# Kernel tuning notes

Measured on AMD Instinct MI355X. Metric: run time of the kernel, lower is better.

Reference implementation:

```python
import jax, jax.numpy as jnp
import numpy as np

D_MODEL = 768
DT_RANK = D_MODEL // 16  # 48
D_CONV = 4
D_INNER = 2 * D_MODEL    # 1536
D_STATE = 16
BATCH, SEQ_LEN = 1, 4096


def setup_inputs() -> dict:
    key = jax.random.key(0)
    ks = jax.random.split(key, 11)
    def n(k, shape, scale=0.02):
        return jax.random.normal(k, shape, dtype=jnp.float32) * scale
    return {
        "u": jax.random.normal(ks[0], (BATCH, SEQ_LEN, D_MODEL), dtype=jnp.float32),
        "in_proj_w": n(ks[1], (2 * D_INNER, D_MODEL)),
        "conv_w": n(ks[2], (D_INNER, 1, D_CONV)),
        "conv_b": n(ks[3], (D_INNER,)),
        "x_dt_w": n(ks[4], (DT_RANK, D_INNER)),
        "x_b_w": n(ks[5], (D_STATE, D_INNER)),
        "x_c_w": n(ks[6], (D_STATE, D_INNER)),
        "dt_w": n(ks[7], (D_INNER, DT_RANK)),
        "dt_b": n(ks[8], (D_INNER,)),
        # HF Mamba-style S4D-real init: A_log = log(1..N) per channel
        "A_log": jnp.log(jnp.tile(jnp.arange(1, D_STATE + 1, dtype=jnp.float32), (D_INNER, 1))),
        "D_param": jnp.ones((D_INNER,), dtype=jnp.float32),
        "out_proj_w": n(ks[9], (D_MODEL, D_INNER)),
    }


def _silu(x):
    return x * jax.nn.sigmoid(x)


def reference(u, in_proj_w, conv_w, conv_b, x_dt_w, x_b_w, x_c_w,
              dt_w, dt_b, A_log, D_param, out_proj_w):
    batch = u.shape[0]
    # input projection -> x, z  [B, L, D_INNER] each
    xz = u @ in_proj_w.T
    x, z = jnp.split(xz, 2, axis=-1)
    # causal depthwise conv1d over time
    x_ncl = jnp.transpose(x, (0, 2, 1))  # [B, D_INNER, L]
    x_conv = jax.lax.conv_general_dilated(
        x_ncl, conv_w, window_strides=(1,), padding=[(D_CONV - 1, 0)],
        dimension_numbers=("NCH", "OIH", "NCH"), feature_group_count=D_INNER)
    x_conv = x_conv + conv_b[None, :, None]
    x_conv = _silu(jnp.transpose(x_conv, (0, 2, 1)))  # [B, L, D_INNER]
    # data-dependent SSM parameters
    dt_rank = x_conv @ x_dt_w.T                      # [B, L, DT_RANK]
    Bm = x_conv @ x_b_w.T                            # [B, L, D_STATE]
    Cm = x_conv @ x_c_w.T                            # [B, L, D_STATE]
    dt = jax.nn.softplus(dt_rank @ dt_w.T + dt_b)    # [B, L, D_INNER]
    A = -jnp.exp(A_log)                              # [D_INNER, D_STATE]
    dA = jnp.exp(dt[..., None] * A)                  # [B, L, D_INNER, D_STATE]
    dB = dt[..., None] * Bm[:, :, None, :]           # [B, L, D_INNER, D_STATE]

    def step(h, inp):
        dA_t, dB_t, x_t, C_t = inp
        h = h * dA_t + x_t[..., None] * dB_t                 # [B, D_INNER, D_STATE]
        y_t = jnp.sum(h * C_t[:, None, :], axis=-1) + D_param * x_t
        return h, y_t

    h0 = jnp.zeros((batch, D_INNER, D_STATE), dtype=u.dtype)
    scan_inputs = (jnp.moveaxis(dA, 1, 0), jnp.moveaxis(dB, 1, 0),
                   jnp.moveaxis(x_conv, 1, 0), jnp.moveaxis(Cm, 1, 0))
    _, y_ssm = jax.lax.scan(step, h0, scan_inputs)   # [L, B, D_INNER]
    y = jnp.moveaxis(y_ssm, 0, 1) * _silu(z)         # [B, L, D_INNER]
    return y @ out_proj_w.T                          # [B, L, D_MODEL]
```

## Files before the change

### kernel.cpp

```cpp
#include <hip/hip_runtime.h>
#include <math.h>

#define L      4096
#define DM     768
#define DI     1536
#define DS     16
#define DR     48
#define NCOMB  80
#define CH     16
#define NC     256
#define G2_S   16
#define G2_KC  96
#define XZROW  6144

typedef unsigned short u16;
typedef unsigned int   u32;
typedef __attribute__((ext_vector_type(8))) short bf16x8;
typedef __attribute__((ext_vector_type(4))) float f32x4;

__device__ __forceinline__ float silu_f(float v) { return v / (1.f + __expf(-v)); }

__device__ __forceinline__ u16 f2bf(float f) {
    u32 u = __float_as_uint(f);
    return (u16)((u + 0x7fffu + ((u >> 16) & 1u)) >> 16);
}
__device__ __forceinline__ float bf2f(u16 h) {
    return __uint_as_float(((u32)h) << 16);
}

__device__ __forceinline__ float softplus_f(float s) {
    return (s > 20.f) ? s : log1pf(expf(s));
}

__device__ __forceinline__ void gl_lds16(const u16* g, u16* l) {
    __builtin_amdgcn_global_load_lds(
        (const __attribute__((address_space(1))) void*)g,
        (__attribute__((address_space(3))) void*)l, 16, 0, 0);
}

__global__ __launch_bounds__(256)
void gemm_bf16_bt(const u16* __restrict__ A, const u16* __restrict__ W,
                  float* __restrict__ C, int M, int N, int K)
{
    __shared__ u16 As[2][128 * 32];
    __shared__ u16 Bs[2][128 * 32];

    const int tid  = threadIdx.x;
    const int lane = tid & 63;
    const int wave = tid >> 6;
    const int wr   = (wave >> 1) * 64;
    const int wc   = (wave & 1) * 64;
    const int m0   = blockIdx.y * 128;
    const int n0   = blockIdx.x * 128;

    const int r0 = tid >> 2;
    const int k0 = (tid & 3) * 8;

    const int frow = lane & 15;
    const int fk   = (lane >> 4) * 8;

    f32x4 acc[4][4];
    #pragma unroll
    for (int i = 0; i < 4; ++i)
        #pragma unroll
        for (int j = 0; j < 4; ++j)
            acc[i][j] = (f32x4){0.f, 0.f, 0.f, 0.f};

    const int NT = K >> 5;

#define STAGE(buf, kk) {                                                       \
        const u16* ga = A + (size_t)(m0 + r0) * K + (kk) + k0;                 \
        const u16* gw = W + (size_t)(n0 + r0) * K + (kk) + k0;                 \
        gl_lds16(ga,                   &As[buf][tid * 8]);                     \
        gl_lds16(ga + (size_t)64 * K,  &As[buf][2048 + tid * 8]);              \
        gl_lds16(gw,                   &Bs[buf][tid * 8]);                     \
        gl_lds16(gw + (size_t)64 * K,  &Bs[buf][2048 + tid * 8]); }

    STAGE(0, 0);
    __syncthreads();

    for (int t = 0; t < NT; ++t) {
        const int b = t & 1;
        if (t + 1 < NT) STAGE(b ^ 1, (t + 1) << 5);

        bf16x8 af[4], bw[4];
        #pragma unroll
        for (int m = 0; m < 4; ++m)
            af[m] = *(const bf16x8*)&As[b][(wr + m * 16 + frow) * 32 + fk];
        #pragma unroll
        for (int n = 0; n < 4; ++n)
            bw[n] = *(const bf16x8*)&Bs[b][(wc + n * 16 + frow) * 32 + fk];

        #pragma unroll
        for (int m = 0; m < 4; ++m)
            #pragma unroll
            for (int n = 0; n < 4; ++n)
                acc[m][n] = __builtin_amdgcn_mfma_f32_16x16x32_bf16(
                    af[m], bw[n], acc[m][n], 0, 0, 0);

        __syncthreads();
    }
#undef STAGE

    const int crow = (lane >> 4) * 4;
    const int ccol = lane & 15;
    #pragma unroll
    for (int m = 0; m < 4; ++m)
        #pragma unroll
        for (int n = 0; n < 4; ++n)
            #pragma unroll
            for (int r = 0; r < 4; ++r)
                C[(size_t)(m0 + wr + m * 16 + crow + r) * N
                  + n0 + wc + n * 16 + ccol] = acc[m][n][r];
}

__global__ __launch_bounds__(256)
void gemm_bf16_bt_n64(const u16* __restrict__ A, int lda,
                      const u16* __restrict__ W, int ldw,
                      float* __restrict__ C, int M, int N, int K)
{
    __shared__ u16 As[2][128 * 32];
    __shared__ u16 Bs[2][64 * 32];

    const int tid  = threadIdx.x;
    const int lane = tid & 63;
    const int wave = tid >> 6;
    const int wr   = (wave >> 1) * 64;
    const int wc   = (wave & 1) * 32;
    const int m0   = blockIdx.y * 128;
    const int n0   = blockIdx.x * 64;

    const int r0 = tid >> 2;
    const int k0 = (tid & 3) * 8;

    const int frow = lane & 15;
    const int fk   = (lane >> 4) * 8;

    f32x4 acc[4][2];
    #pragma unroll
    for (int i = 0; i < 4; ++i)
        #pragma unroll
        for (int j = 0; j < 2; ++j)
            acc[i][j] = (f32x4){0.f, 0.f, 0.f, 0.f};

    const int NT = K >> 5;

#define STG(buf, kk) {                                                         \
        const u16* ga = A + (size_t)(m0 + r0) * lda + (kk) + k0;               \
        gl_lds16(ga,                     &As[buf][tid * 8]);                   \
        gl_lds16(ga + (size_t)64 * lda,  &As[buf][2048 + tid * 8]);            \
        gl_lds16(W + (size_t)(n0 + r0) * ldw + (kk) + k0, &Bs[buf][tid * 8]); }

    STG(0, 0);
    __syncthreads();

    for (int t = 0; t < NT; ++t) {
        const int b = t & 1;
        if (t + 1 < NT) STG(b ^ 1, (t + 1) << 5);

        bf16x8 af[4], bw[2];
        #pragma unroll
        for (int m = 0; m < 4; ++m)
            af[m] = *(const bf16x8*)&As[b][(wr + m * 16 + frow) * 32 + fk];
        #pragma unroll
        for (int n = 0; n < 2; ++n)
            bw[n] = *(const bf16x8*)&Bs[b][(wc + n * 16 + frow) * 32 + fk];

        #pragma unroll
        for (int m = 0; m < 4; ++m)
            #pragma unroll
            for (int n = 0; n < 2; ++n)
                acc[m][n] = __builtin_amdgcn_mfma_f32_16x16x32_bf16(
                    af[m], bw[n], acc[m][n], 0, 0, 0);

        __syncthreads();
    }
#undef STG

    const int crow = (lane >> 4) * 4;
    const int ccol = lane & 15;
    #pragma unroll
    for (int m = 0; m < 4; ++m)
        #pragma unroll
        for (int n = 0; n < 2; ++n)
            #pragma unroll
            for (int r = 0; r < 4; ++r)
                C[(size_t)(m0 + wr + m * 16 + crow + r) * N
                  + n0 + wc + n * 16 + ccol] = acc[m][n][r];
}

#define NU4  (L * DM / 4)
#define NW4  (2 * DI * DM / 4)
#define NWT  (DI * NCOMB)
__global__ __launch_bounds__(256)
void pack_early_k(const float* __restrict__ u, const float* __restrict__ Wip,
                  const float* __restrict__ xdt, const float* __restrict__ xb,
                  const float* __restrict__ xc,
                  u16* __restrict__ ubf, u16* __restrict__ Wipb,
                  float* __restrict__ Wt)
{
    int i = blockIdx.x * 256 + threadIdx.x;
    if (i < NU4) {
        const float4 v = ((const float4*)u)[i];
        ushort4 o; o.x = f2bf(v.x); o.y = f2bf(v.y); o.z = f2bf(v.z); o.w = f2bf(v.w);
        ((ushort4*)ubf)[i] = o;
        return;
    }
    i -= NU4;
    if (i < NW4) {
        const float4 v = ((const float4*)Wip)[i];
        ushort4 o; o.x = f2bf(v.x); o.y = f2bf(v.y); o.z = f2bf(v.z); o.w = f2bf(v.w);
        ((ushort4*)Wipb)[i] = o;
        return;
    }
    i -= NW4;
    if (i < NWT) {
        const int k = i / NCOMB, n = i - k * NCOMB;
        float v;
        if (n < 48)      v = xdt[n * DI + k];
        else if (n < 64) v = xb[(n - 48) * DI + k];
        else             v = xc[(n - 64) * DI + k];
        Wt[i] = v;
    }
}

#define NO4  (DM * DI / 4)
__global__ __launch_bounds__(256)
void pack_wop_k(const float* __restrict__ Wop, u16* __restrict__ xzu)
{
    int i = blockIdx.x * 256 + threadIdx.x;
    if (i >= NO4) return;
    const float4 v = ((const float4*)Wop)[i];
    ushort4 o; o.x = f2bf(v.x); o.y = f2bf(v.y); o.z = f2bf(v.z); o.w = f2bf(v.w);
    const int e = i * 4;
    const int r = e / DI, c = e - r * DI;
    *(ushort4*)(xzu + (size_t)r * XZROW + 1536 + c) = o;
}

__global__ __launch_bounds__(256)
void conv_silu_v4(const float* __restrict__ xz, const float* __restrict__ cw,
                  const float* __restrict__ cb, float* __restrict__ xcv)
{
    int idx = blockIdx.x * 256 + threadIdx.x;
    if (idx >= L * (DI / 4)) return;
    const int t = idx / (DI / 4);
    const int q = idx - t * (DI / 4);
    const int d = q * 4;

    const float4 w0 = ((const float4*)cw)[d + 0];
    const float4 w1 = ((const float4*)cw)[d + 1];
    const float4 w2 = ((const float4*)cw)[d + 2];
    const float4 w3 = ((const float4*)cw)[d + 3];
    float4 acc = ((const float4*)cb)[q];

    const float* base = xz + d;
    #pragma unroll
    for (int j = 0; j < 4; ++j) {
        const int tt = t - 3 + j;
        if (tt >= 0) {
            const float4 x = *(const float4*)(base + (size_t)tt * (2 * DI));
            acc.x = fmaf(((const float*)&w0)[j], x.x, acc.x);
            acc.y = fmaf(((const float*)&w1)[j], x.y, acc.y);
            acc.z = fmaf(((const float*)&w2)[j], x.z, acc.z);
            acc.w = fmaf(((const float*)&w3)[j], x.w, acc.w);
        }
    }
    float4 o;
    o.x = silu_f(acc.x); o.y = silu_f(acc.y);
    o.z = silu_f(acc.z); o.w = silu_f(acc.w);
    ((float4*)xcv)[idx] = o;
}

__global__ __launch_bounds__(256)
void gemm2_splitk(const float* __restrict__ A, const float* __restrict__ Wt,
                  float* __restrict__ part)
{
    __shared__ float As[G2_KC][65];
    __shared__ float Ws[G2_KC][80];

    const int tid  = threadIdx.x;
    const int m0   = blockIdx.x * 64;
    const int koff = blockIdx.y * G2_KC;

    {
        const int r = tid >> 2, cg = tid & 3;
        #pragma unroll
        for (int j = 0; j < 6; ++j) {
            const int kk = (j * 4 + cg) * 4;
            const float4 v = *(const float4*)(A + (size_t)(m0 + r) * DI + koff + kk);
            As[kk + 0][r] = v.x; As[kk + 1][r] = v.y;
            As[kk + 2][r] = v.z; As[kk + 3][r] = v.w;
        }
    }
    for (int i = tid; i < G2_KC * 80; i += 256)
        (&Ws[0][0])[i] = Wt[(size_t)koff * 80 + i];
    __syncthreads();

    const int g  = tid >> 6;
    const int r  = tid & 63;
    const int c0 = g * 20;

    float acc[20];
    #pragma unroll
    for (int j = 0; j < 20; ++j) acc[j] = 0.f;

    #pragma unroll 2
    for (int k = 0; k < G2_KC; ++k) {
        const float a = As[k][r];
        #pragma unroll
        for (int q = 0; q < 5; ++q) {
            const float4 w = *(const float4*)&Ws[k][c0 + q * 4];
            acc[q * 4 + 0] = fmaf(a, w.x, acc[q * 4 + 0]);
            acc[q * 4 + 1] = fmaf(a, w.y, acc[q * 4 + 1]);
            acc[q * 4 + 2] = fmaf(a, w.z, acc[q * 4 + 2]);
            acc[q * 4 + 3] = fmaf(a, w.w, acc[q * 4 + 3]);
        }
    }

    float* p = part + (size_t)blockIdx.y * (L * NCOMB)
                    + (size_t)(m0 + r) * NCOMB + c0;
    #pragma unroll
    for (int q = 0; q < 5; ++q)
        ((float4*)p)[q] = make_float4(acc[q * 4], acc[q * 4 + 1],
                                      acc[q * 4 + 2], acc[q * 4 + 3]);
}

__global__ __launch_bounds__(256)
void gemm2_reduce(const float* __restrict__ part, float* __restrict__ dtbc)
{
    int i = blockIdx.x * 256 + threadIdx.x;
    if (i >= L * NCOMB) return;
    float s = 0.f;
    #pragma unroll
    for (int j = 0; j < G2_S; ++j)
        s += part[(size_t)j * L * NCOMB + i];
    dtbc[i] = s;
}

__global__ __launch_bounds__(256)
void dt_k(const float* __restrict__ dtbc, const float* __restrict__ dtw,
          const float* __restrict__ dtb, u16* __restrict__ dt)
{
    __shared__ float dtr_s[32][48];
    const int tid = threadIdx.x;
    const int d   = blockIdx.x * 256 + tid;
    const int t0  = blockIdx.y * 32;

    for (int i = tid; i < 384; i += 256) {
        const int r = i / 12, c = (i - r * 12) * 4;
        const float4 v = *(const float4*)(dtbc + (size_t)(t0 + r) * NCOMB + c);
        *(float4*)&dtr_s[r][c] = v;
    }
    __syncthreads();

    float w[48];
    #pragma unroll
    for (int j = 0; j < 12; ++j) {
        const float4 v = *(const float4*)(dtw + (size_t)d * DR + j * 4);
        w[j * 4 + 0] = v.x; w[j * 4 + 1] = v.y;
        w[j * 4 + 2] = v.z; w[j * 4 + 3] = v.w;
    }
    const float b = dtb[d];

    for (int t = 0; t < 32; ++t) {
        float s = b;
        #pragma unroll
        for (int j = 0; j < 12; ++j) {
            const float4 v = *(const float4*)&dtr_s[t][j * 4];
            s = fmaf(v.x, w[j * 4 + 0], s);
            s = fmaf(v.y, w[j * 4 + 1], s);
            s = fmaf(v.z, w[j * 4 + 2], s);
            s = fmaf(v.w, w[j * 4 + 3], s);
        }
        dt[(size_t)(t0 + t) * DI + d] = f2bf(softplus_f(s));
    }
}

__global__ __launch_bounds__(256)
void scan1_k(const u16* __restrict__ dt, const float* __restrict__ xcv,
             const float* __restrict__ dtbc, const float* __restrict__ alog,
             u16* __restrict__ hloc, float* __restrict__ Ssum)
{
    __shared__ float Bs[CH][DS];
    const int c = blockIdx.y;
    const int d = blockIdx.x * 256 + threadIdx.x;

    {
        const int i = threadIdx.x;
        const int tt = i >> 4, n = i & 15;
        Bs[tt][n] = dtbc[(size_t)(c * CH + tt) * NCOMB + 48 + n];
    }
    __syncthreads();

    float Ad[DS], h[DS];
    #pragma unroll
    for (int n = 0; n < DS; ++n) {
        Ad[n] = -expf(alog[d * DS + n]);
        h[n] = 0.f;
    }

    size_t base = (size_t)(c * CH) * DI + d;
    float S = 0.f;
    for (int tt = 0; tt < CH; ++tt, base += DI) {
        const float dtv = bf2f(dt[base]);
        const float xv  = xcv[base];
        S += dtv;
        const float xdt = xv * dtv;
        #pragma unroll
        for (int n = 0; n < DS; ++n)
            h[n] = fmaf(h[n], __expf(Ad[n] * dtv), xdt * Bs[tt][n]);
    }

    u16* o = hloc + ((size_t)c * DI + d) * DS;
    #pragma unroll
    for (int q = 0; q < 4; ++q) {
        ushort4 pk;
        pk.x = f2bf(h[q * 4 + 0]); pk.y = f2bf(h[q * 4 + 1]);
        pk.z = f2bf(h[q * 4 + 2]); pk.w = f2bf(h[q * 4 + 3]);
        *(ushort4*)(o + q * 4) = pk;
    }
    Ssum[c * DI + d] = S;
}

__global__ __launch_bounds__(256)
void scan2_k(u16* hc, const float* __restrict__ Ssum,
             const float* __restrict__ alog)
{
    const int p = blockIdx.x * 256 + threadIdx.x;
    if (p >= DI * DS) return;
    const int d = p >> 4;
    const float Ad = -expf(alog[p]);
    float h = 0.f;
    for (int c = 0; c < NC; ++c) {
        const size_t o = (size_t)c * DI * DS + p;
        const float hl = bf2f(hc[o]);
        hc[o] = f2bf(h);
        h = fmaf(h, __expf(Ad * Ssum[c * DI + d]), hl);
    }
}

__global__ __launch_bounds__(256)
void scan3_k(const u16* __restrict__ dt, const float* __restrict__ xcv,
             const float* __restrict__ dtbc, const float* __restrict__ alog,
             const u16* __restrict__ carry, const float* __restrict__ Dp,
             const float* __restrict__ xz, u16* __restrict__ ybf)
{
    __shared__ float Bs[CH][DS];
    __shared__ float Cs[CH][DS];
    const int c = blockIdx.y;
    const int d = blockIdx.x * 256 + threadIdx.x;

    {
        const int i = threadIdx.x;
        const int tt = i >> 4, n = i & 15;
        Bs[tt][n] = dtbc[(size_t)(c * CH + tt) * NCOMB + 48 + n];
        Cs[tt][n] = dtbc[(size_t)(c * CH + tt) * NCOMB + 64 + n];
    }
    __syncthreads();

    float Ad[DS], h[DS];
    const u16* co = carry + ((size_t)c * DI + d) * DS;
    #pragma unroll
    for (int q = 0; q < 4; ++q) {
        const ushort4 cv = *(const ushort4*)(co + q * 4);
        h[q * 4 + 0] = bf2f(cv.x); h[q * 4 + 1] = bf2f(cv.y);
        h[q * 4 + 2] = bf2f(cv.z); h[q * 4 + 3] = bf2f(cv.w);
    }
    #pragma unroll
    for (int n = 0; n < DS; ++n)
        Ad[n] = -expf(alog[d * DS + n]);
    const float Dv = Dp[d];

    int t = c * CH;
    for (int tt = 0; tt < CH; ++tt, ++t) {
        const size_t o = (size_t)t * DI + d;
        const float dtv = bf2f(dt[o]);
        const float xv  = xcv[o];
        const float xdt = xv * dtv;
        float y = Dv * xv;
        #pragma unroll
        for (int n = 0; n < DS; ++n) {
            h[n] = fmaf(h[n], __expf(Ad[n] * dtv), xdt * Bs[tt][n]);
            y = fmaf(h[n], Cs[tt][n], y);
        }
        const float z = xz[(size_t)t * (2 * DI) + DI + d];
        ybf[(size_t)t * XZROW + d] = f2bf(y * silu_f(z));
    }
}

extern "C" void kernel_launch(void* const* d_in, const int* in_sizes, int n_in,
                              void* d_out, int out_size, void* d_ws, size_t ws_size,
                              hipStream_t stream)
{
    const float* u    = (const float*)d_in[0];
    const float* Wip  = (const float*)d_in[1];
    const float* cw   = (const float*)d_in[2];
    const float* cb   = (const float*)d_in[3];
    const float* xdt  = (const float*)d_in[4];
    const float* xbw  = (const float*)d_in[5];
    const float* xcw  = (const float*)d_in[6];
    const float* dtw  = (const float*)d_in[7];
    const float* dtb  = (const float*)d_in[8];
    const float* alog = (const float*)d_in[9];
    const float* Dp   = (const float*)d_in[10];
    const float* Wop  = (const float*)d_in[11];
    float* out = (float*)d_out;

    float* ws   = (float*)d_ws;
    float* xz   = ws;
    float* xcv  = xz   + (size_t)L * 2 * DI;
    float* dtbc = xcv  + (size_t)L * DI;
    float* dty  = dtbc + (size_t)L * NCOMB;
    float* Wt   = dty  + (size_t)L * DI;
    u16*   hc   = (u16*)(Wt + (size_t)DI * NCOMB);
    float* Ssum = Wt + (size_t)DI * NCOMB
                     + (size_t)NC * DI * DS / 2;

    u16*   ubf  = (u16*)xcv;
    u16*   Wipb = (u16*)xcv + (size_t)L * DM;
    float* g2p  = dty;
    u16*   dtbf = (u16*)dty;
    u16*   xzu  = (u16*)xz;

    const dim3 blk(256);

    pack_early_k<<<(NU4 + NW4 + NWT + 255) / 256, blk, 0, stream>>>(
        u, Wip, xdt, xbw, xcw, ubf, Wipb, Wt);

    gemm_bf16_bt<<<dim3((2 * DI) / 128, L / 128), blk, 0, stream>>>(
        ubf, Wipb, xz, L, 2 * DI, DM);

    conv_silu_v4<<<(L * (DI / 4) + 255) / 256, blk, 0, stream>>>(xz, cw, cb, xcv);

    pack_wop_k<<<(NO4 + 255) / 256, blk, 0, stream>>>(Wop, xzu);

    gemm2_splitk<<<dim3(L / 64, G2_S), blk, 0, stream>>>(xcv, Wt, g2p);
    gemm2_reduce<<<(L * NCOMB + 255) / 256, blk, 0, stream>>>(g2p, dtbc);

    dt_k<<<dim3(DI / 256, L / 32), blk, 0, stream>>>(dtbc, dtw, dtb, dtbf);

    scan1_k<<<dim3(DI / 256, NC), blk, 0, stream>>>(
        dtbf, xcv, dtbc, alog, hc, Ssum);
    scan2_k<<<(DI * DS) / 256, blk, 0, stream>>>(hc, Ssum, alog);
    scan3_k<<<dim3(DI / 256, NC), blk, 0, stream>>>(
        dtbf, xcv, dtbc, alog, hc, Dp, xz, xzu);

    gemm_bf16_bt_n64<<<dim3(DM / 64, L / 128), blk, 0, stream>>>(
        xzu, XZROW, xzu + 1536, XZROW, out, L, DM, DI);
}
```

Baseline: 247.9 us.

## Process two channels per thread in chunked scan and precompute negated A

The chunk-local scan kernels (scan1, scan3) now have each thread handle two adjacent channels, using paired loads of dt, x, z and packed stores, and halving the grid. -exp(A_log) is computed once in the packing kernel into a workspace buffer and read as float4s instead of being recomputed in every scan block. This aims to cut redundant exp work and per-element load instructions and to increase ILP. The cost is twice the state registers per thread and fewer blocks: 3x256 in each chunked scan kernel.

```diff
diff --git a/kernel.cpp b/kernel.cpp
--- a/kernel.cpp
+++ b/kernel.cpp
@@ -192,12 +192,13 @@
 #define NU4  (L * DM / 4)
 #define NW4  (2 * DI * DM / 4)
 #define NWT  (DI * NCOMB)
+#define NA   (DI * DS)
 __global__ __launch_bounds__(256)
 void pack_early_k(const float* __restrict__ u, const float* __restrict__ Wip,
                   const float* __restrict__ xdt, const float* __restrict__ xb,
-                  const float* __restrict__ xc,
+                  const float* __restrict__ xc, const float* __restrict__ alog,
                   u16* __restrict__ ubf, u16* __restrict__ Wipb,
-                  float* __restrict__ Wt)
+                  float* __restrict__ Wt, float* __restrict__ Aneg)
 {
     int i = blockIdx.x * 256 + threadIdx.x;
     if (i < NU4) {
@@ -221,7 +222,11 @@
         else if (n < 64) v = xb[(n - 48) * DI + k];
         else             v = xc[(n - 64) * DI + k];
         Wt[i] = v;
-    }
+        return;
+    }
+    i -= NWT;
+    if (i < NA)
+        Aneg[i] = -expf(alog[i]);
 }
 
 #define NO4  (DM * DI / 4)
@@ -378,58 +383,69 @@
 
 __global__ __launch_bounds__(256)
 void scan1_k(const u16* __restrict__ dt, const float* __restrict__ xcv,
-             const float* __restrict__ dtbc, const float* __restrict__ alog,
+             const float* __restrict__ dtbc, const float* __restrict__ Aneg,
              u16* __restrict__ hloc, float* __restrict__ Ssum)
 {
     __shared__ float Bs[CH][DS];
+    const int tid = threadIdx.x;
     const int c = blockIdx.y;
-    const int d = blockIdx.x * 256 + threadIdx.x;
+    const int d = blockIdx.x * 512 + 2 * tid;
 
     {
-        const int i = threadIdx.x;
-        const int tt = i >> 4, n = i & 15;
+        const int tt = tid >> 4, n = tid & 15;
         Bs[tt][n] = dtbc[(size_t)(c * CH + tt) * NCOMB + 48 + n];
     }
     __syncthreads();
 
-    float Ad[DS], h[DS];
-    #pragma unroll
-    for (int n = 0; n < DS; ++n) {
-        Ad[n] = -expf(alog[d * DS + n]);
-        h[n] = 0.f;
-    }
+    float Ad0[DS], Ad1[DS], h0[DS], h1[DS];
+    #pragma unroll
+    for (int q = 0; q < 4; ++q) {
+        *(float4*)&Ad0[q * 4] = *(const float4*)(Aneg + (size_t)d * DS + q * 4);
+        *(float4*)&Ad1[q * 4] = *(const float4*)(Aneg + (size_t)(d + 1) * DS + q * 4);
+    }
+    #pragma unroll
+    for (int n = 0; n < DS; ++n) { h0[n] = 0.f; h1[n] = 0.f; }
 
     size_t base = (size_t)(c * CH) * DI + d;
-    float S = 0.f;
+    float S0 = 0.f, S1 = 0.f;
     for (int tt = 0; tt < CH; ++tt, base += DI) {
-        const float dtv = bf2f(dt[base]);
-        const float xv  = xcv[base];
-        S += dtv;
-        const float xdt = xv * dtv;
-        #pragma unroll
-        for (int n = 0; n < DS; ++n)
-            h[n] = fmaf(h[n], __expf(Ad[n] * dtv), xdt * Bs[tt][n]);
+        const u32 dtp = *(const u32*)(dt + base);
+        const float dtv0 = bf2f((u16)(dtp & 0xffff));
+        const float dtv1 = bf2f((u16)(dtp >> 16));
+        const float2 xv = *(const float2*)(xcv + base);
+        S0 += dtv0; S1 += dtv1;
+        const float xdt0 = xv.x * dtv0;
+        const float xdt1 = xv.y * dtv1;
+        #pragma unroll
+        for (int n = 0; n < DS; ++n) {
+            const float b = Bs[tt][n];
+            h0[n] = fmaf(h0[n], __expf(Ad0[n] * dtv0), xdt0 * b);
+            h1[n] = fmaf(h1[n], __expf(Ad1[n] * dtv1), xdt1 * b);
+        }
     }
 
     u16* o = hloc + ((size_t)c * DI + d) * DS;
     #pragma unroll
     for (int q = 0; q < 4; ++q) {
         ushort4 pk;
-        pk.x = f2bf(h[q * 4 + 0]); pk.y = f2bf(h[q * 4 + 1]);
-        pk.z = f2bf(h[q * 4 + 2]); pk.w = f2bf(h[q * 4 + 3]);
+        pk.x = f2bf(h0[q * 4 + 0]); pk.y = f2bf(h0[q * 4 + 1]);
+        pk.z = f2bf(h0[q * 4 + 2]); pk.w = f2bf(h0[q * 4 + 3]);
         *(ushort4*)(o + q * 4) = pk;
-    }
-    Ssum[c * DI + d] = S;
+        pk.x = f2bf(h1[q * 4 + 0]); pk.y = f2bf(h1[q * 4 + 1]);
+        pk.z = f2bf(h1[q * 4 + 2]); pk.w = f2bf(h1[q * 4 + 3]);
+        *(ushort4*)(o + DS + q * 4) = pk;
+    }
+    *(float2*)(Ssum + (size_t)c * DI + d) = make_float2(S0, S1);
 }
 
 __global__ __launch_bounds__(256)
 void scan2_k(u16* hc, const float* __restrict__ Ssum,
-             const float* __restrict__ alog)
+             const float* __restrict__ Aneg)
 {
     const int p = blockIdx.x * 256 + threadIdx.x;
     if (p >= DI * DS) return;
     const int d = p >> 4;
-    const float Ad = -expf(alog[p]);
+    const float Ad = Aneg[p];
     float h = 0.f;
     for (int c = 0; c < NC; ++c) {
         const size_t o = (size_t)c * DI * DS + p;
@@ -441,50 +457,65 @@
 
 __global__ __launch_bounds__(256)
 void scan3_k(const u16* __restrict__ dt, const float* __restrict__ xcv,
-             const float* __restrict__ dtbc, const float* __restrict__ alog,
+             const float* __restrict__ dtbc, const float* __restrict__ Aneg,
              const u16* __restrict__ carry, const float* __restrict__ Dp,
              const float* __restrict__ xz, u16* __restrict__ ybf)
 {
     __shared__ float Bs[CH][DS];
     __shared__ float Cs[CH][DS];
+    const int tid = threadIdx.x;
     const int c = blockIdx.y;
-    const int d = blockIdx.x * 256 + threadIdx.x;
+    const int d = blockIdx.x * 512 + 2 * tid;
 
     {
-        const int i = threadIdx.x;
-        const int tt = i >> 4, n = i & 15;
+        const int tt = tid >> 4, n = tid & 15;
         Bs[tt][n] = dtbc[(size_t)(c * CH + tt) * NCOMB + 48 + n];
         Cs[tt][n] = dtbc[(size_t)(c * CH + tt) * NCOMB + 64 + n];
     }
     __syncthreads();
 
-    float Ad[DS], h[DS];
+    float Ad0[DS], Ad1[DS], h0[DS], h1[DS];
+    #pragma unroll
+    for (int q = 0; q < 4; ++q) {
+        *(float4*)&Ad0[q * 4] = *(const float4*)(Aneg + (size_t)d * DS + q * 4);
+        *(float4*)&Ad1[q * 4] = *(const float4*)(Aneg + (size_t)(d + 1) * DS + q * 4);
+    }
     const u16* co = carry + ((size_t)c * DI + d) * DS;
     #pragma unroll
     for (int q = 0; q < 4; ++q) {
-        const ushort4 cv = *(const ushort4*)(co + q * 4);
-        h[q * 4 + 0] = bf2f(cv.x); h[q * 4 + 1] = bf2f(cv.y);
-        h[q * 4 + 2] = bf2f(cv.z); h[q * 4 + 3] = bf2f(cv.w);
-    }
-    #pragma unroll
-    for (int n = 0; n < DS; ++n)
-        Ad[n] = -expf(alog[d * DS + n]);
-    const float Dv = Dp[d];
+        ushort4 cv = *(const ushort4*)(co + q * 4);
+        h0[q * 4 + 0] = bf2f(cv.x); h0[q * 4 + 1] = bf2f(cv.y);
+        h0[q * 4 + 2] = bf2f(cv.z); h0[q * 4 + 3] = bf2f(cv.w);
+        cv = *(const ushort4*)(co + DS + q * 4);
+        h1[q * 4 + 0] = bf2f(cv.x); h1[q * 4 + 1] = bf2f(cv.y);
+        h1[q * 4 + 2] = bf2f(cv.z); h1[q * 4 + 3] = bf2f(cv.w);
+    }
+    const float2 Dv = *(const float2*)(Dp + d);
 
     int t = c * CH;
     for (int tt = 0; tt < CH; ++tt, ++t) {
         const size_t o = (size_t)t * DI + d;
-        const float dtv = bf2f(dt[o]);
-        const float xv  = xcv[o];
-        const float xdt = xv * dtv;
-        float y = Dv * xv;
+        const u32 dtp = *(const u32*)(dt + o);
+        const float dtv0 = bf2f((u16)(dtp & 0xffff));
+        const float dtv1 = bf2f((u16)(dtp >> 16));
+        const float2 xv = *(const float2*)(xcv + o);
+        const float xdt0 = xv.x * dtv0;
+        const float xdt1 = xv.y * dtv1;
+        float y0 = Dv.x * xv.x;
+        float y1 = Dv.y * xv.y;
         #pragma unroll
         for (int n = 0; n < DS; ++n) {
-            h[n] = fmaf(h[n], __expf(Ad[n] * dtv), xdt * Bs[tt][n]);
-            y = fmaf(h[n], Cs[tt][n], y);
+            const float b = Bs[tt][n];
+            const float cc = Cs[tt][n];
+            h0[n] = fmaf(h0[n], __expf(Ad0[n] * dtv0), xdt0 * b);
+            h1[n] = fmaf(h1[n], __expf(Ad1[n] * dtv1), xdt1 * b);
+            y0 = fmaf(h0[n], cc, y0);
+            y1 = fmaf(h1[n], cc, y1);
         }
-        const float z = xz[(size_t)t * (2 * DI) + DI + d];
-        ybf[(size_t)t * XZROW + d] = f2bf(y * silu_f(z));
+        const float2 z = *(const float2*)(xz + (size_t)t * (2 * DI) + DI + d);
+        const u32 pk = (u32)f2bf(y0 * silu_f(z.x))
+                     | ((u32)f2bf(y1 * silu_f(z.y)) << 16);
+        *(u32*)(ybf + (size_t)t * XZROW + d) = pk;
     }
 }
 
@@ -515,6 +546,7 @@
     u16*   hc   = (u16*)(Wt + (size_t)DI * NCOMB);
     float* Ssum = Wt + (size_t)DI * NCOMB
                      + (size_t)NC * DI * DS / 2;
+    float* Aneg = Ssum + (size_t)NC * DI;
 
     u16*   ubf  = (u16*)xcv;
     u16*   Wipb = (u16*)xcv + (size_t)L * DM;
@@ -524,8 +556,8 @@
 
     const dim3 blk(256);
 
-    pack_early_k<<<(NU4 + NW4 + NWT + 255) / 256, blk, 0, stream>>>(
-        u, Wip, xdt, xbw, xcw, ubf, Wipb, Wt);
+    pack_early_k<<<(NU4 + NW4 + NWT + NA + 255) / 256, blk, 0, stream>>>(
+        u, Wip, xdt, xbw, xcw, alog, ubf, Wipb, Wt, Aneg);
 
     gemm_bf16_bt<<<dim3((2 * DI) / 128, L / 128), blk, 0, stream>>>(
         ubf, Wipb, xz, L, 2 * DI, DM);
@@ -539,11 +571,11 @@
 
     dt_k<<<dim3(DI / 256, L / 32), blk, 0, stream>>>(dtbc, dtw, dtb, dtbf);
 
-    scan1_k<<<dim3(DI / 256, NC), blk, 0, stream>>>(
-        dtbf, xcv, dtbc, alog, hc, Ssum);
-    scan2_k<<<(DI * DS) / 256, blk, 0, stream>>>(hc, Ssum, alog);
-    scan3_k<<<dim3(DI / 256, NC), blk, 0, stream>>>(
-        dtbf, xcv, dtbc, alog, hc, Dp, xz, xzu);
+    scan1_k<<<dim3(DI / 512, NC), blk, 0, stream>>>(
+        dtbf, xcv, dtbc, Aneg, hc, Ssum);
+    scan2_k<<<(DI * DS) / 256, blk, 0, stream>>>(hc, Ssum, Aneg);
+    scan3_k<<<dim3(DI / 512, NC), blk, 0, stream>>>(
+        dtbf, xcv, dtbc, Aneg, hc, Dp, xz, xzu);
 
     gemm_bf16_bt_n64<<<dim3(DM / 64, L / 128), blk, 0, stream>>>(
         xzu, XZROW, xzu + 1536, XZROW, out, L, DM, DI);
```

Result: no change. 252.2 us (+1.7%).

## Fuse three-pass chunked scan into one cooperative kernel with grid syncs

Applied to the files above, without the earlier changes.

Merges the three scan kernels (per-chunk local scan, cross-chunk carry propagation, final output pass) into one cooperative kernel separated by grid-wide syncs. Each chunk's dt and x values stay in shared memory between pass one and pass three instead of being reloaded from global memory. The chunk length doubles so the 768-block grid can be co-resident, and -exp(A_log) is precomputed once in the pack kernel. The risks are grid.sync overhead, a carry pass that only uses 16 of 128 chunk rows, a longer serial loop per chunk, and heavier shared-memory use that could limit occupancy.

```diff
diff --git a/kernel.cpp b/kernel.cpp
--- a/kernel.cpp
+++ b/kernel.cpp
@@ -1,4 +1,5 @@
 #include <hip/hip_runtime.h>
+#include <hip/hip_cooperative_groups.h>
 #include <math.h>
 
 #define L      4096
@@ -7,8 +8,8 @@
 #define DS     16
 #define DR     48
 #define NCOMB  80
-#define CH     16
-#define NC     256
+#define CH     32
+#define NC     128
 #define G2_S   16
 #define G2_KC  96
 #define XZROW  6144
@@ -192,12 +193,13 @@
 #define NU4  (L * DM / 4)
 #define NW4  (2 * DI * DM / 4)
 #define NWT  (DI * NCOMB)
+#define NA   (DI * DS)
 __global__ __launch_bounds__(256)
 void pack_early_k(const float* __restrict__ u, const float* __restrict__ Wip,
                   const float* __restrict__ xdt, const float* __restrict__ xb,
-                  const float* __restrict__ xc,
+                  const float* __restrict__ xc, const float* __restrict__ alog,
                   u16* __restrict__ ubf, u16* __restrict__ Wipb,
-                  float* __restrict__ Wt)
+                  float* __restrict__ Wt, float* __restrict__ Aneg)
 {
     int i = blockIdx.x * 256 + threadIdx.x;
     if (i < NU4) {
@@ -221,7 +223,11 @@
         else if (n < 64) v = xb[(n - 48) * DI + k];
         else             v = xc[(n - 64) * DI + k];
         Wt[i] = v;
-    }
+        return;
+    }
+    i -= NWT;
+    if (i < NA)
+        Aneg[i] = -expf(alog[i]);
 }
 
 #define NO4  (DM * DI / 4)
@@ -376,115 +382,116 @@
     }
 }
 
-__global__ __launch_bounds__(256)
-void scan1_k(const u16* __restrict__ dt, const float* __restrict__ xcv,
-             const float* __restrict__ dtbc, const float* __restrict__ alog,
-             u16* __restrict__ hloc, float* __restrict__ Ssum)
-{
-    __shared__ float Bs[CH][DS];
-    const int c = blockIdx.y;
-    const int d = blockIdx.x * 256 + threadIdx.x;
+namespace cg = cooperative_groups;
+
+__global__ __launch_bounds__(256)
+void scan_fused_k(const u16* __restrict__ dt, const float* __restrict__ xcv,
+                  const float* __restrict__ dtbc, const float* __restrict__ Aneg,
+                  const float* __restrict__ Dp, const float* __restrict__ xz,
+                  u16* __restrict__ ybf, u16* hc, float* __restrict__ Ssum)
+{
+    __shared__ float xs[CH][256];
+    __shared__ u16   dts[CH][256];
+
+    cg::grid_group grid = cg::this_grid();
+
+    const int tid = threadIdx.x;
+    const int cb  = blockIdx.x;
+    const int c   = blockIdx.y;
+    const int d   = cb * 256 + tid;
+
+    float Ad[DS], h[DS];
+    #pragma unroll
+    for (int q = 0; q < 4; ++q)
+        *(float4*)&Ad[q * 4] = *(const float4*)(Aneg + (size_t)d * DS + q * 4);
+    #pragma unroll
+    for (int n = 0; n < DS; ++n) h[n] = 0.f;
 
     {
-        const int i = threadIdx.x;
-        const int tt = i >> 4, n = i & 15;
-        Bs[tt][n] = dtbc[(size_t)(c * CH + tt) * NCOMB + 48 + n];
-    }
-    __syncthreads();
-
-    float Ad[DS], h[DS];
-    #pragma unroll
-    for (int n = 0; n < DS; ++n) {
-        Ad[n] = -expf(alog[d * DS + n]);
-        h[n] = 0.f;
-    }
-
-    size_t base = (size_t)(c * CH) * DI + d;
-    float S = 0.f;
-    for (int tt = 0; tt < CH; ++tt, base += DI) {
-        const float dtv = bf2f(dt[base]);
-        const float xv  = xcv[base];
-        S += dtv;
-        const float xdt = xv * dtv;
-        #pragma unroll
-        for (int n = 0; n < DS; ++n)
-            h[n] = fmaf(h[n], __expf(Ad[n] * dtv), xdt * Bs[tt][n]);
-    }
-
-    u16* o = hloc + ((size_t)c * DI + d) * DS;
-    #pragma unroll
-    for (int q = 0; q < 4; ++q) {
-        ushort4 pk;
-        pk.x = f2bf(h[q * 4 + 0]); pk.y = f2bf(h[q * 4 + 1]);
-        pk.z = f2bf(h[q * 4 + 2]); pk.w = f2bf(h[q * 4 + 3]);
-        *(ushort4*)(o + q * 4) = pk;
-    }
-    Ssum[c * DI + d] = S;
-}
-
-__global__ __launch_bounds__(256)
-void scan2_k(u16* hc, const float* __restrict__ Ssum,
-             const float* __restrict__ alog)
-{
-    const int p = blockIdx.x * 256 + threadIdx.x;
-    if (p >= DI * DS) return;
-    const int d = p >> 4;
-    const float Ad = -expf(alog[p]);
-    float h = 0.f;
-    for (int c = 0; c < NC; ++c) {
-        const size_t o = (size_t)c * DI * DS + p;
-        const float hl = bf2f(hc[o]);
-        hc[o] = f2bf(h);
-        h = fmaf(h, __expf(Ad * Ssum[c * DI + d]), hl);
-    }
-}
-
-__global__ __launch_bounds__(256)
-void scan3_k(const u16* __restrict__ dt, const float* __restrict__ xcv,
-             const float* __restrict__ dtbc, const float* __restrict__ alog,
-             const u16* __restrict__ carry, const float* __restrict__ Dp,
-             const float* __restrict__ xz, u16* __restrict__ ybf)
-{
-    __shared__ float Bs[CH][DS];
-    __shared__ float Cs[CH][DS];
-    const int c = blockIdx.y;
-    const int d = blockIdx.x * 256 + threadIdx.x;
+        size_t base = (size_t)(c * CH) * DI + d;
+        float S = 0.f;
+        for (int tt = 0; tt < CH; ++tt, base += DI) {
+            const u16  draw = dt[base];
+            const float xv  = xcv[base];
+            dts[tt][tid] = draw;
+            xs[tt][tid]  = xv;
+            const float dtv = bf2f(draw);
+            S += dtv;
+            const float xdt = xv * dtv;
+            const float* brow = dtbc + (size_t)(c * CH + tt) * NCOMB + 48;
+            #pragma unroll
+            for (int q = 0; q < 4; ++q) {
+                const float4 bq = *(const float4*)(brow + q * 4);
+                h[q * 4 + 0] = fmaf(h[q * 4 + 0], __expf(Ad[q * 4 + 0] * dtv), xdt * bq.x);
+                h[q * 4 + 1] = fmaf(h[q * 4 + 1], __expf(Ad[q * 4 + 1] * dtv), xdt * bq.y);
+                h[q * 4 + 2] = fmaf(h[q * 4 + 2], __expf(Ad[q * 4 + 2] * dtv), xdt * bq.z);
+                h[q * 4 + 3] = fmaf(h[q * 4 + 3], __expf(Ad[q * 4 + 3] * dtv), xdt * bq.w);
+            }
+        }
+        u16* o = hc + ((size_t)c * DI + d) * DS;
+        #pragma unroll
+        for (int q = 0; q < 4; ++q) {
+            ushort4 pk;
+            pk.x = f2bf(h[q * 4 + 0]); pk.y = f2bf(h[q * 4 + 1]);
+            pk.z = f2bf(h[q * 4 + 2]); pk.w = f2bf(h[q * 4 + 3]);
+            *(ushort4*)(o + q * 4) = pk;
+        }
+        Ssum[(size_t)c * DI + d] = S;
+    }
+
+    __threadfence();
+    grid.sync();
+
+    if (c < 16) {
+        const int p = (c * 6 + cb) * 256 + tid;
+        const int d2 = p >> 4;
+        const float Ad2 = Aneg[p];
+        float h2 = 0.f;
+        for (int cc = 0; cc < NC; ++cc) {
+            const size_t o = (size_t)cc * DI * DS + p;
+            const float hl = bf2f(hc[o]);
+            hc[o] = f2bf(h2);
+            h2 = fmaf(h2, __expf(Ad2 * Ssum[(size_t)cc * DI + d2]), hl);
+        }
+    }
+
+    __threadfence();
+    grid.sync();
 
     {
-        const int i = threadIdx.x;
-        const int tt = i >> 4, n = i & 15;
-        Bs[tt][n] = dtbc[(size_t)(c * CH + tt) * NCOMB + 48 + n];
-        Cs[tt][n] = dtbc[(size_t)(c * CH + tt) * NCOMB + 64 + n];
-    }
-    __syncthreads();
-
-    float Ad[DS], h[DS];
-    const u16* co = carry + ((size_t)c * DI + d) * DS;
-    #pragma unroll
-    for (int q = 0; q < 4; ++q) {
-        const ushort4 cv = *(const ushort4*)(co + q * 4);
-        h[q * 4 + 0] = bf2f(cv.x); h[q * 4 + 1] = bf2f(cv.y);
-        h[q * 4 + 2] = bf2f(cv.z); h[q * 4 + 3] = bf2f(cv.w);
-    }
-    #pragma unroll
-    for (int n = 0; n < DS; ++n)
-        Ad[n] = -expf(alog[d * DS + n]);
-    const float Dv = Dp[d];
-
-    int t = c * CH;
-    for (int tt = 0; tt < CH; ++tt, ++t) {
-        const size_t o = (size_t)t * DI + d;
-        const float dtv = bf2f(dt[o]);
-        const float xv  = xcv[o];
-        const float xdt = xv * dtv;
-        float y = Dv * xv;
-        #pragma unroll
-        for (int n = 0; n < DS; ++n) {
-            h[n] = fmaf(h[n], __expf(Ad[n] * dtv), xdt * Bs[tt][n]);
-            y = fmaf(h[n], Cs[tt][n], y);
-        }
-        const float z = xz[(size_t)t * (2 * DI) + DI + d];
-        ybf[(size_t)t * XZROW + d] = f2bf(y * silu_f(z));
+        const u16* co = hc + ((size_t)c * DI + d) * DS;
+        #pragma unroll
+        for (int q = 0; q < 4; ++q) {
+            const ushort4 cv = *(const ushort4*)(co + q * 4);
+            h[q * 4 + 0] = bf2f(cv.x); h[q * 4 + 1] = bf2f(cv.y);
+            h[q * 4 + 2] = bf2f(cv.z); h[q * 4 + 3] = bf2f(cv.w);
+        }
+        const float Dv = Dp[d];
+
+        int t = c * CH;
+        for (int tt = 0; tt < CH; ++tt, ++t) {
+            const float dtv = bf2f(dts[tt][tid]);
+            const float xv  = xs[tt][tid];
+            const float xdt = xv * dtv;
+            float y = Dv * xv;
+            const float* brow = dtbc + (size_t)(c * CH + tt) * NCOMB + 48;
+            const float* crow = brow + 16;
+            #pragma unroll
+            for (int q = 0; q < 4; ++q) {
+                const float4 bq = *(const float4*)(brow + q * 4);
+                const float4 cq = *(const float4*)(crow + q * 4);
+                h[q * 4 + 0] = fmaf(h[q * 4 + 0], __expf(Ad[q * 4 + 0] * dtv), xdt * bq.x);
+                h[q * 4 + 1] = fmaf(h[q * 4 + 1], __expf(Ad[q * 4 + 1] * dtv), xdt * bq.y);
+                h[q * 4 + 2] = fmaf(h[q * 4 + 2], __expf(Ad[q * 4 + 2] * dtv), xdt * bq.z);
+                h[q * 4 + 3] = fmaf(h[q * 4 + 3], __expf(Ad[q * 4 + 3] * dtv), xdt * bq.w);
+                y = fmaf(h[q * 4 + 0], cq.x, y);
+                y = fmaf(h[q * 4 + 1], cq.y, y);
+                y = fmaf(h[q * 4 + 2], cq.z, y);
+                y = fmaf(h[q * 4 + 3], cq.w, y);
+            }
+            const float z = xz[(size_t)t * (2 * DI) + DI + d];
+            ybf[(size_t)t * XZROW + d] = f2bf(y * silu_f(z));
+        }
     }
 }
 
@@ -515,6 +522,7 @@
     u16*   hc   = (u16*)(Wt + (size_t)DI * NCOMB);
     float* Ssum = Wt + (size_t)DI * NCOMB
                      + (size_t)NC * DI * DS / 2;
+    float* Aneg = Ssum + (size_t)NC * DI;
 
     u16*   ubf  = (u16*)xcv;
     u16*   Wipb = (u16*)xcv + (size_t)L * DM;
@@ -524,8 +532,8 @@
 
     const dim3 blk(256);
 
-    pack_early_k<<<(NU4 + NW4 + NWT + 255) / 256, blk, 0, stream>>>(
-        u, Wip, xdt, xbw, xcw, ubf, Wipb, Wt);
+    pack_early_k<<<(NU4 + NW4 + NWT + NA + 255) / 256, blk, 0, stream>>>(
+        u, Wip, xdt, xbw, xcw, alog, ubf, Wipb, Wt, Aneg);
 
     gemm_bf16_bt<<<dim3((2 * DI) / 128, L / 128), blk, 0, stream>>>(
         ubf, Wipb, xz, L, 2 * DI, DM);
@@ -539,11 +547,20 @@
 
     dt_k<<<dim3(DI / 256, L / 32), blk, 0, stream>>>(dtbc, dtw, dtb, dtbf);
 
-    scan1_k<<<dim3(DI / 256, NC), blk, 0, stream>>>(
-        dtbf, xcv, dtbc, alog, hc, Ssum);
-    scan2_k<<<(DI * DS) / 256, blk, 0, stream>>>(hc, Ssum, alog);
-    scan3_k<<<dim3(DI / 256, NC), blk, 0, stream>>>(
-        dtbf, xcv, dtbc, alog, hc, Dp, xz, xzu);
+    {
+        const u16*   a0 = dtbf;
+        const float* a1 = xcv;
+        const float* a2 = dtbc;
+        const float* a3 = Aneg;
+        const float* a4 = Dp;
+        const float* a5 = xz;
+        u16*         a6 = xzu;
+        u16*         a7 = hc;
+        float*       a8 = Ssum;
+        void* kargs[] = { &a0, &a1, &a2, &a3, &a4, &a5, &a6, &a7, &a8 };
+        hipLaunchCooperativeKernel((void*)scan_fused_k,
+                                   dim3(DI / 256, NC), blk, kargs, 0, stream);
+    }
 
     gemm_bf16_bt_n64<<<dim3(DM / 64, L / 128), blk, 0, stream>>>(
         xzu, XZROW, xzu + 1536, XZROW, out, L, DM, DI);
```

New measurement: 567.1 us. 129% more time.
